# Optimization experiments

Hardware: AMD Instinct MI355X
Metric: run time of the kernel (lower is better)

The kernel has to match this reference:

```python
import jax, jax.numpy as jnp
import numpy as np

# SGCN (AsynSpiGCN) internals are not in the source; reconstructed as a standard
# LIF spiking-GCN: per time step, spikes propagate along edges weighted by
# edge_attr (gather src -> scatter-add dst), membrane potential decays with
# decay_alpha, neurons fire above threshold unless refractory, reset to v_r.
V_REST = 0.0
V_R = 0.0
SPEED = 1.0
THRESH = 0.5
REFRAC = 2.0
DECAY = 0.8
T_STEPS = 8
BETA = 0.5

N_NODES = 50000
N_EDGES = 800000
IN_DIM = 256
HID_DIM = 128


def setup_inputs() -> dict:
    key = jax.random.key(0)
    k1, k2, k3, k4, k5 = jax.random.split(key, 5)
    x = jax.random.normal(k1, (N_NODES, IN_DIM), dtype=jnp.float32)
    spike_node = jax.random.randint(k2, (N_NODES,), 0, 2, dtype=jnp.int32)
    edge_index = jax.random.randint(k3, (2, N_EDGES), 0, N_NODES, dtype=jnp.int32)
    node_indices = jnp.arange(N_NODES, dtype=jnp.int32)
    edge_attr = jax.random.uniform(k4, (N_EDGES,), dtype=jnp.float32)
    W = jax.random.normal(k5, (IN_DIM, HID_DIM), dtype=jnp.float32) * 0.05
    b = jnp.zeros((HID_DIM,), dtype=jnp.float32)
    return {"x": x, "spike_node": spike_node, "edge_index": edge_index,
            "node_indices": node_indices, "edge_attr": edge_attr, "W": W, "b": b}


def reference(x, spike_node, edge_index, node_indices, edge_attr, W, b):
    N = x.shape[0]
    # Linear projection + per-feature min-max standardization over nodes (dim 0)
    h = x @ W + b
    mn = h.min(axis=0, keepdims=True)
    mx = h.max(axis=0, keepdims=True)
    h = (h - mn) / (mx - mn + 1e-6)

    src, dst = edge_index[0], edge_index[1]
    v0 = jnp.full_like(h, V_REST)            # membrane potential [N, H]
    ref0 = jnp.zeros_like(h)                 # refractory counters [N, H]
    s0 = jnp.broadcast_to(spike_node.astype(h.dtype)[:, None], h.shape)

    def step(carry, _):
        v, ref, s = carry
        msg = s[src] * edge_attr[:, None]                      # [E, H] gather
        agg = jax.ops.segment_sum(msg, dst, num_segments=N)    # [N, H] scatter-add
        v = DECAY * v + SPEED * h + agg
        can_fire = ref <= 0
        spk = ((v >= THRESH) & can_fire).astype(h.dtype)
        v = jnp.where(spk > 0, V_R, v)
        ref = jnp.where(spk > 0, REFRAC, jnp.maximum(ref - 1.0, 0.0))
        return (v, ref, spk), spk

    (vT, _, _), spike_matrix = jax.lax.scan(step, (v0, ref0, s0), None, length=T_STEPS)
    fusion_tensor = h + BETA * vT
    return fusion_tensor, spike_matrix
```

## Files before the change

kernel.cpp:

```cpp
#include <hip/hip_runtime.h>
#include <cstdint>

#define N_NODES 50000
#define N_EDGES 800000
#define IN_DIM  256
#define HID     128
#define T_STEPS 8

#define AG_LOAD(p)     __hip_atomic_load((p), __ATOMIC_RELAXED, __HIP_MEMORY_SCOPE_AGENT)
#define AG_STORE(p, v) __hip_atomic_store((p), (v), __ATOMIC_RELAXED, __HIP_MEMORY_SCOPE_AGENT)
#define AG_ADD(p, v)   __hip_atomic_fetch_add((p), (v), __ATOMIC_RELAXED, __HIP_MEMORY_SCOPE_AGENT)
#define AG_MIN(p, v)   __hip_atomic_fetch_min((p), (v), __ATOMIC_RELAXED, __HIP_MEMORY_SCOPE_AGENT)
#define AG_MAX(p, v)   __hip_atomic_fetch_max((p), (v), __ATOMIC_RELAXED, __HIP_MEMORY_SCOPE_AGENT)

typedef unsigned long long u64;

static __device__ __forceinline__ unsigned int enc_f(float f) {
    unsigned int u = __float_as_uint(f);
    return (u & 0x80000000u) ? ~u : (u | 0x80000000u);
}
static __device__ __forceinline__ float dec_f(unsigned int u) {
    unsigned int b = (u & 0x80000000u) ? (u ^ 0x80000000u) : ~u;
    return __uint_as_float(b);
}

static __device__ __forceinline__ void fbar(int* bar, int nblk, int t) {
    int* flags = bar;
    int* go    = bar + 1900;
    __syncthreads();
    if (blockIdx.x == 0) {
        if (threadIdx.x == 0) AG_STORE(&flags[0], t);
        for (;;) {
            int ok = 1;
            for (int i = (int)threadIdx.x; i < nblk; i += 256)
                ok &= (AG_LOAD(&flags[i]) >= t);
            if (__syncthreads_and(ok)) break;
            __builtin_amdgcn_s_sleep(1);
        }
        if (threadIdx.x == 0) AG_STORE(go, t);
    } else {
        if (threadIdx.x == 0) {
            AG_STORE(&flags[blockIdx.x], t);
            while (AG_LOAD(go) < t) __builtin_amdgcn_s_sleep(4);
        }
        __syncthreads();
    }
}

template<int TNPB, int TNSLOT, int TECAP, int TBCAP, int TMINW>
__global__ __launch_bounds__(256, TMINW) void k_mega3(
    const float* __restrict__ x,
    const int*   __restrict__ spike_node,
    const int*   __restrict__ esrc,
    const int*   __restrict__ edst,
    const float* __restrict__ eattr,
    const float* __restrict__ W,
    const float* __restrict__ b,
    int* cnt, int4* bucket,
    unsigned int* mn_e, unsigned int* mx_e,
    uint32_t* sbA, uint32_t* sbB,
    float* __restrict__ out,
    int* bar, int nblk)
{
    constexpr int GEMMW = 4096 + TNPB * 36 + 64;
    constexpr int POOLW = (TECAP * 6 > GEMMW) ? TECAP * 6 : GEMMW;

    __shared__ int      lrp[TNPB + 1];
    __shared__ uint32_t pool[POOLW];
    __shared__ uint32_t sbw[TNPB][4];

    int*      ed_src_l  = (int*)pool;
    float*    ed_attr_l = (float*)(pool + TECAP);
    uint32_t* ed_wds    = pool + 2 * TECAP;
    float*    Ws        = (float*)pool;
    float*    xs        = (float*)(pool + 4096);
    float*    red_mn    = (float*)pool;
    float*    red_mx    = (float*)(pool + 1024);
    int*      cnt_l     = (int*)sbw;

    const int tid = threadIdx.x;
    const int bid = blockIdx.x;
    const int g   = tid >> 5, ln = tid & 31;
    const int n0  = bid * TNPB;
    const int ncnt = min(TNPB, N_NODES - n0);
    const int w = ln >> 3, shb = (ln & 7) * 4;
    const size_t NH = (size_t)N_NODES * HID;

    for (int i = tid; i < ncnt; i += 256) {
        uint32_t f = spike_node[n0 + i] ? 0xFFFFFFFFu : 0u;
        u64 ff = (u64)f | ((u64)f << 32);
        AG_STORE((u64*)&sbA[(size_t)(n0 + i) * 4], ff);
        AG_STORE((u64*)&sbA[(size_t)(n0 + i) * 4 + 2], ff);
    }

    for (int e = bid * 256 + tid; e < N_EDGES; e += nblk * 256) {
        int d = edst[e];
        int p = AG_ADD(&cnt[d], 1);
        if (p < TBCAP) {
            u64* qp = (u64*)&bucket[(size_t)d * TBCAP + p];
            u64 a  = (u64)(unsigned int)e | ((u64)(unsigned int)esrc[e] << 32);
            u64 bq = (u64)__float_as_uint(eattr[e]);
            AG_STORE(qp, a);
            AG_STORE(qp + 1, bq);
        }
    }

    float4 hs[TNSLOT], vs[TNSLOT];
    uint32_t rcs[TNSLOT], nibs[TNSLOT];
    #pragma unroll
    for (int s = 0; s < TNSLOT; ++s) hs[s] = make_float4(0.f, 0.f, 0.f, 0.f);
    int xoff[TNSLOT];
    #pragma unroll
    for (int s = 0; s < TNSLOT; ++s) xoff[s] = min(s * 8 + g, TNPB - 1) * 36;

    for (int kc = 0; kc < IN_DIM; kc += 32) {
        __syncthreads();
        for (int idx = tid; idx < TNPB * 8; idx += 256) {
            int node = idx >> 3, q = idx & 7;
            int row = min(n0 + node, N_NODES - 1);
            *(float4*)&xs[node * 36 + q * 4] =
                *(const float4*)(x + (size_t)row * IN_DIM + kc + q * 4);
        }
        for (int idx = tid; idx < 1024; idx += 256) {
            int r = idx >> 5, c = idx & 31;
            *(float4*)&Ws[r * 128 + c * 4] =
                *(const float4*)(W + (size_t)(kc + r) * HID + c * 4);
        }
        __syncthreads();
        #pragma unroll 4
        for (int k = 0; k < 32; ++k) {
            float4 wf = *(float4*)&Ws[k * 128 + ln * 4];
            #pragma unroll
            for (int s = 0; s < TNSLOT; ++s) {
                float xv = xs[xoff[s] + k];
                hs[s].x = __fmaf_rn(xv, wf.x, hs[s].x);
                hs[s].y = __fmaf_rn(xv, wf.y, hs[s].y);
                hs[s].z = __fmaf_rn(xv, wf.z, hs[s].z);
                hs[s].w = __fmaf_rn(xv, wf.w, hs[s].w);
            }
        }
    }
    {
        float4 bv = *(const float4*)(b + ln * 4);
        float lmn[4], lmx[4];
        #pragma unroll
        for (int c = 0; c < 4; ++c) { lmn[c] = INFINITY; lmx[c] = -INFINITY; }
        #pragma unroll
        for (int s = 0; s < TNSLOT; ++s) {
            hs[s].x = __fadd_rn(hs[s].x, bv.x);
            hs[s].y = __fadd_rn(hs[s].y, bv.y);
            hs[s].z = __fadd_rn(hs[s].z, bv.z);
            hs[s].w = __fadd_rn(hs[s].w, bv.w);
            lmn[0] = fminf(lmn[0], hs[s].x); lmx[0] = fmaxf(lmx[0], hs[s].x);
            lmn[1] = fminf(lmn[1], hs[s].y); lmx[1] = fmaxf(lmx[1], hs[s].y);
            lmn[2] = fminf(lmn[2], hs[s].z); lmx[2] = fmaxf(lmx[2], hs[s].z);
            lmn[3] = fminf(lmn[3], hs[s].w); lmx[3] = fmaxf(lmx[3], hs[s].w);
        }
        __syncthreads();
        #pragma unroll
        for (int c = 0; c < 4; ++c) {
            red_mn[g * 128 + ln * 4 + c] = lmn[c];
            red_mx[g * 128 + ln * 4 + c] = lmx[c];
        }
        __syncthreads();
        if (tid < 128) {
            float mnv = red_mn[tid], mxv = red_mx[tid];
            #pragma unroll
            for (int r = 1; r < 8; ++r) {
                mnv = fminf(mnv, red_mn[r * 128 + tid]);
                mxv = fmaxf(mxv, red_mx[r * 128 + tid]);
            }
            AG_MIN(&mn_e[tid], enc_f(mnv));
            AG_MAX(&mx_e[tid], enc_f(mxv));
        }
        __syncthreads();
    }

    fbar(bar, nblk, 1);

    if (tid < ncnt) cnt_l[tid] = min(AG_LOAD(&cnt[n0 + tid]), TBCAP);
    __syncthreads();
    if (tid == 0) {
        int run = 0;
        for (int i = 0; i < ncnt; ++i) { lrp[i] = run; run += cnt_l[i]; }
        lrp[ncnt] = run;
    }
    __syncthreads();
    const int etot  = lrp[ncnt];
    const bool inlds = (etot <= TECAP);

    {
        float mn0 = dec_f(AG_LOAD(&mn_e[ln * 4 + 0]));
        float mn1 = dec_f(AG_LOAD(&mn_e[ln * 4 + 1]));
        float mn2 = dec_f(AG_LOAD(&mn_e[ln * 4 + 2]));
        float mn3 = dec_f(AG_LOAD(&mn_e[ln * 4 + 3]));
        float dd0 = __fadd_rn(__fsub_rn(dec_f(AG_LOAD(&mx_e[ln * 4 + 0])), mn0), 1e-6f);
        float dd1 = __fadd_rn(__fsub_rn(dec_f(AG_LOAD(&mx_e[ln * 4 + 1])), mn1), 1e-6f);
        float dd2 = __fadd_rn(__fsub_rn(dec_f(AG_LOAD(&mx_e[ln * 4 + 2])), mn2), 1e-6f);
        float dd3 = __fadd_rn(__fsub_rn(dec_f(AG_LOAD(&mx_e[ln * 4 + 3])), mn3), 1e-6f);
        #pragma unroll
        for (int s = 0; s < TNSLOT; ++s) {
            hs[s].x = __fdiv_rn(__fsub_rn(hs[s].x, mn0), dd0);
            hs[s].y = __fdiv_rn(__fsub_rn(hs[s].y, mn1), dd1);
            hs[s].z = __fdiv_rn(__fsub_rn(hs[s].z, mn2), dd2);
            hs[s].w = __fdiv_rn(__fsub_rn(hs[s].w, mn3), dd3);
        }
    }
    #pragma unroll
    for (int s = 0; s < TNSLOT; ++s) { vs[s] = make_float4(0.f,0.f,0.f,0.f); rcs[s] = 0u; }

    if (inlds) {
        for (int m = tid >> 6; m < ncnt; m += 4) {
            int l = tid & 63;
            int lbeg = lrp[m];
            int c = lrp[m + 1] - lbeg;
            if (c <= 0) continue;
            const u64* brow = (const u64*)&bucket[(size_t)(n0 + m) * TBCAP];
            if (c <= 64) {
                int key = 0x7FFFFFFF, sv = 0, av = 0;
                if (l < c) {
                    u64 a  = AG_LOAD(brow + 2 * l);
                    u64 bq = AG_LOAD(brow + 2 * l + 1);
                    key = (int)(unsigned int)a;
                    sv  = (int)(unsigned int)(a >> 32);
                    av  = (int)(unsigned int)bq;
                }
                #pragma unroll
                for (int k = 2; k <= 64; k <<= 1) {
                    for (int j = k >> 1; j > 0; j >>= 1) {
                        int pk2 = __shfl_xor(key, j);
                        int ps  = __shfl_xor(sv, j);
                        int pa  = __shfl_xor(av, j);
                        bool lower = (l & j) == 0;
                        bool asc   = (l & k) == 0;
                        bool take  = (lower == asc) ? (pk2 < key) : (pk2 > key);
                        if (take) { key = pk2; sv = ps; av = pa; }
                    }
                }
                if (l < c) {
                    ed_src_l[lbeg + l]  = sv;
                    ed_attr_l[lbeg + l] = __int_as_float(av);
                }
            } else if (l == 0) {
                for (int i = 0; i < c; ++i) {
                    u64 a  = AG_LOAD(brow + 2 * i);
                    u64 bq = AG_LOAD(brow + 2 * i + 1);
                    int ke  = (int)(unsigned int)a;
                    int svv = (int)(unsigned int)(a >> 32);
                    int avv = (int)(unsigned int)bq;
                    int mm = i - 1;
                    while (mm >= 0 && (int)ed_wds[lbeg + mm] > ke) {
                        ed_wds[lbeg + mm + 1]    = ed_wds[lbeg + mm];
                        ed_src_l[lbeg + mm + 1]  = ed_src_l[lbeg + mm];
                        ed_attr_l[lbeg + mm + 1] = ed_attr_l[lbeg + mm];
                        --mm;
                    }
                    ed_wds[lbeg + mm + 1]    = (uint32_t)ke;
                    ed_src_l[lbeg + mm + 1]  = svv;
                    ed_attr_l[lbeg + mm + 1] = __int_as_float(avv);
                }
            }
        }
    } else {
        for (int m = tid >> 6; m < ncnt; m += 4) {
            int l = tid & 63;
            int c = lrp[m + 1] - lrp[m];
            if (c <= 1) continue;
            u64* brow = (u64*)&bucket[(size_t)(n0 + m) * TBCAP];
            if (c <= 64) {
                int key = 0x7FFFFFFF, sv = 0, av = 0;
                if (l < c) {
                    u64 a  = AG_LOAD(brow + 2 * l);
                    u64 bq = AG_LOAD(brow + 2 * l + 1);
                    key = (int)(unsigned int)a;
                    sv  = (int)(unsigned int)(a >> 32);
                    av  = (int)(unsigned int)bq;
                }
                #pragma unroll
                for (int k = 2; k <= 64; k <<= 1) {
                    for (int j = k >> 1; j > 0; j >>= 1) {
                        int pk2 = __shfl_xor(key, j);
                        int ps  = __shfl_xor(sv, j);
                        int pa  = __shfl_xor(av, j);
                        bool lower = (l & j) == 0;
                        bool asc   = (l & k) == 0;
                        bool take  = (lower == asc) ? (pk2 < key) : (pk2 > key);
                        if (take) { key = pk2; sv = ps; av = pa; }
                    }
                }
                if (l < c) {
                    u64 a = (u64)(unsigned int)key | ((u64)(unsigned int)sv << 32);
                    AG_STORE(brow + 2 * l, a);
                    AG_STORE(brow + 2 * l + 1, (u64)(unsigned int)av);
                }
            } else if (l == 0) {
                for (int i = 1; i < c; ++i) {
                    u64 ka = AG_LOAD(brow + 2 * i);
                    u64 kb = AG_LOAD(brow + 2 * i + 1);
                    int ke = (int)(unsigned int)ka;
                    int mm = i - 1;
                    while (mm >= 0) {
                        u64 ma = AG_LOAD(brow + 2 * mm);
                        if ((int)(unsigned int)ma <= ke) break;
                        AG_STORE(brow + 2 * mm + 2, ma);
                        AG_STORE(brow + 2 * mm + 3, AG_LOAD(brow + 2 * mm + 1));
                        --mm;
                    }
                    AG_STORE(brow + 2 * mm + 2, ka);
                    AG_STORE(brow + 2 * mm + 3, kb);
                }
            }
        }
    }
    __syncthreads();
    for (int i = tid; i < ncnt * 2; i += 256) ((u64*)sbw)[i] = 0ull;

    for (int t = 0; t < T_STEPS; ++t) {
        const uint32_t* cur = (t & 1) ? sbB : sbA;
        uint32_t*       nxt = (t & 1) ? sbA : sbB;
        if (t > 0) fbar(bar, nblk, 1 + t);

        if (inlds) {
            for (int i = tid; i < etot; i += 256) {
                u64* sp = (u64*)&cur[(size_t)ed_src_l[i] * 4];
                u64 lo = AG_LOAD(sp);
                u64 hi = AG_LOAD(sp + 1);
                uint4 wv;
                wv.x = (uint32_t)lo; wv.y = (uint32_t)(lo >> 32);
                wv.z = (uint32_t)hi; wv.w = (uint32_t)(hi >> 32);
                *(uint4*)&ed_wds[i * 4] = wv;
            }
        }
        __syncthreads();

        if (t > 0) {
            #pragma unroll
            for (int s = 0; s < TNSLOT; ++s) {
                int m = s * 8 + g;
                if (m < ncnt) {
                    uint32_t nb4 = nibs[s];
                    size_t idx = (size_t)(n0 + m) * HID + ln * 4;
                    *(float4*)&out[NH + (size_t)(t - 1) * NH + idx] = make_float4(
                        (nb4 & 1u) ? 1.0f : 0.0f, (nb4 & 2u) ? 1.0f : 0.0f,
                        (nb4 & 4u) ? 1.0f : 0.0f, (nb4 & 8u) ? 1.0f : 0.0f);
                }
            }
        }

        #pragma unroll
        for (int s = 0; s < TNSLOT; ++s) {
            int m = s * 8 + g;
            if (m < ncnt) {
                float ag0 = 0.f, ag1 = 0.f, ag2 = 0.f, ag3 = 0.f;
                if (inlds) {
                    int lb = lrp[m], le = lrp[m + 1];
                    for (int i = lb; i < le; ++i) {
                        uint32_t u = ed_wds[i * 4 + w];
                        float a = ed_attr_l[i];
                        uint32_t bits = (u >> shb) & 0xFu;
                        ag0 = __fadd_rn(ag0, (bits & 1u) ? a : 0.f);
                        ag1 = __fadd_rn(ag1, (bits & 2u) ? a : 0.f);
                        ag2 = __fadd_rn(ag2, (bits & 4u) ? a : 0.f);
                        ag3 = __fadd_rn(ag3, (bits & 8u) ? a : 0.f);
                    }
                } else {
                    int c = lrp[m + 1] - lrp[m];
                    const u64* brow = (const u64*)&bucket[(size_t)(n0 + m) * TBCAP];
                    for (int i = 0; i < c; ++i) {
                        u64 a  = AG_LOAD(brow + 2 * i);
                        u64 bq = AG_LOAD(brow + 2 * i + 1);
                        int srcn = (int)(unsigned int)(a >> 32);
                        float av = __uint_as_float((unsigned int)bq);
                        uint32_t u = AG_LOAD((uint32_t*)&cur[(size_t)srcn * 4 + w]);
                        uint32_t bits = (u >> shb) & 0xFu;
                        ag0 = __fadd_rn(ag0, (bits & 1u) ? av : 0.f);
                        ag1 = __fadd_rn(ag1, (bits & 2u) ? av : 0.f);
                        ag2 = __fadd_rn(ag2, (bits & 4u) ? av : 0.f);
                        ag3 = __fadd_rn(ag3, (bits & 8u) ? av : 0.f);
                    }
                }

                float hv[4] = {hs[s].x, hs[s].y, hs[s].z, hs[s].w};
                float vv[4] = {vs[s].x, vs[s].y, vs[s].z, vs[s].w};
                float ag[4] = {ag0, ag1, ag2, ag3};
                float vf[4];
                uint32_t rcu = rcs[s], rcn = 0u, nib = 0u;
                #pragma unroll
                for (int q = 0; q < 4; ++q) {
                    float vn = __fadd_rn(__fadd_rn(__fmul_rn(0.8f, vv[q]), hv[q]), ag[q]);
                    uint32_t rc = (rcu >> (8 * q)) & 0xFFu;
                    bool spk = (vn >= 0.5f) && (rc == 0u);
                    vf[q] = spk ? 0.0f : vn;
                    uint32_t rnew = spk ? 2u : (rc > 0u ? rc - 1u : 0u);
                    rcn |= rnew << (8 * q);
                    nib |= (spk ? 1u : 0u) << q;
                }
                vs[s] = make_float4(vf[0], vf[1], vf[2], vf[3]);
                rcs[s] = rcn;
                nibs[s] = nib;
                atomicOr(&sbw[m][w], nib << shb);
            }
        }
        __syncthreads();
        for (int i = tid; i < ncnt * 2; i += 256) {
            AG_STORE((u64*)&nxt[(size_t)n0 * 4] + i, ((u64*)sbw)[i]);
            ((u64*)sbw)[i] = 0ull;
        }
    }

    #pragma unroll
    for (int s = 0; s < TNSLOT; ++s) {
        int m = s * 8 + g;
        if (m < ncnt) {
            uint32_t nb4 = nibs[s];
            size_t idx = (size_t)(n0 + m) * HID + ln * 4;
            *(float4*)&out[NH + (size_t)(T_STEPS - 1) * NH + idx] = make_float4(
                (nb4 & 1u) ? 1.0f : 0.0f, (nb4 & 2u) ? 1.0f : 0.0f,
                (nb4 & 4u) ? 1.0f : 0.0f, (nb4 & 8u) ? 1.0f : 0.0f);
            *(float4*)&out[idx] = make_float4(
                __fadd_rn(hs[s].x, __fmul_rn(0.5f, vs[s].x)),
                __fadd_rn(hs[s].y, __fmul_rn(0.5f, vs[s].y)),
                __fadd_rn(hs[s].z, __fmul_rn(0.5f, vs[s].z)),
                __fadd_rn(hs[s].w, __fmul_rn(0.5f, vs[s].w)));
        }
    }
}

__global__ void k_count(const int* __restrict__ dst, int* __restrict__ counts) {
    int e = blockIdx.x * blockDim.x + threadIdx.x;
    if (e < N_EDGES) atomicAdd(&counts[dst[e]], 1);
}

__global__ void k_scan1(const int* __restrict__ counts, int* __restrict__ row_tmp,
                        int* __restrict__ blocksum) {
    __shared__ int sh[256];
    int t = threadIdx.x, i = blockIdx.x * 256 + t;
    int c = (i < N_NODES) ? counts[i] : 0;
    sh[t] = c; __syncthreads();
    for (int off = 1; off < 256; off <<= 1) {
        int val = (t >= off) ? sh[t - off] : 0;
        __syncthreads();
        sh[t] += val;
        __syncthreads();
    }
    if (i < N_NODES) row_tmp[i] = sh[t] - c;
    if (t == 255) blocksum[blockIdx.x] = sh[255];
}

__global__ void k_scan2(const int* __restrict__ blocksum, int* __restrict__ blockoff,
                        int nb, int* __restrict__ row_ptr) {
    if (threadIdx.x == 0) {
        int acc = 0;
        for (int b = 0; b < nb; ++b) { blockoff[b] = acc; acc += blocksum[b]; }
        row_ptr[N_NODES] = acc;
    }
}

__global__ void k_scan3(const int* __restrict__ row_tmp, const int* __restrict__ blockoff,
                        int* __restrict__ row_ptr) {
    int i = blockIdx.x * blockDim.x + threadIdx.x;
    if (i < N_NODES) row_ptr[i] = row_tmp[i] + blockoff[i >> 8];
}

__global__ void k_fill(const int* __restrict__ dst, const int* __restrict__ src,
                       const float* __restrict__ attr,
                       const int* __restrict__ row_ptr, int* __restrict__ cursor,
                       int* __restrict__ eid, int2* __restrict__ edata) {
    int e = blockIdx.x * blockDim.x + threadIdx.x;
    if (e >= N_EDGES) return;
    int d = dst[e];
    int p = row_ptr[d] + atomicAdd(&cursor[d], 1);
    eid[p]   = e;
    edata[p] = make_int2(src[e], __float_as_int(attr[e]));
}

__global__ __launch_bounds__(256) void k_bsort(const int* __restrict__ row_ptr,
                                               int* __restrict__ eid,
                                               int2* __restrict__ edata) {
    int node = blockIdx.x * 4 + (threadIdx.x >> 6);
    int l = threadIdx.x & 63;
    int beg = row_ptr[node], end = row_ptr[node + 1], cnt = end - beg;
    if (cnt <= 1) return;
    if (cnt <= 64) {
        int key = 0x7FFFFFFF, sv = 0, av = 0;
        if (l < cnt) { key = eid[beg + l]; int2 d = edata[beg + l]; sv = d.x; av = d.y; }
        #pragma unroll
        for (int k = 2; k <= 64; k <<= 1) {
            for (int j = k >> 1; j > 0; j >>= 1) {
                int pk = __shfl_xor(key, j);
                int ps = __shfl_xor(sv, j);
                int pa = __shfl_xor(av, j);
                bool lower = (l & j) == 0;
                bool asc   = (l & k) == 0;
                bool take = ((lower == asc)) ? (pk < key) : (pk > key);
                if (take) { key = pk; sv = ps; av = pa; }
            }
        }
        if (l < cnt) { eid[beg + l] = key; edata[beg + l] = make_int2(sv, av); }
    } else if (l == 0) {
        for (int i = beg + 1; i < end; ++i) {
            int ke = eid[i]; int2 kd = edata[i];
            int m = i - 1;
            while (m >= beg && eid[m] > ke) {
                eid[m+1] = eid[m]; edata[m+1] = edata[m]; --m;
            }
            eid[m+1] = ke; edata[m+1] = kd;
        }
    }
}

__global__ __launch_bounds__(256) void k_gemm(const float* __restrict__ x,
                                              const float* __restrict__ W,
                                              const float* __restrict__ b,
                                              float* __restrict__ h,
                                              unsigned int* __restrict__ mn_e,
                                              unsigned int* __restrict__ mx_e) {
    __shared__ float Ws[32 * 128];
    __shared__ float xs[64 * 36];
    __shared__ float red_mn[8 * 128];
    __shared__ float red_mx[8 * 128];
    const int tid = threadIdx.x;
    const int n0 = blockIdx.x * 64;
    const int jt = tid & 31, nt = tid >> 5;
    const int j0 = jt * 4;

    float acc[8][4];
    #pragma unroll
    for (int a = 0; a < 8; ++a)
        #pragma unroll
        for (int c = 0; c < 4; ++c) acc[a][c] = 0.0f;

    const int ldn = tid >> 2;
    const int kq  = (tid & 3) * 8;
    const int xrow = (n0 + ldn < N_NODES) ? (n0 + ldn) : (N_NODES - 1);
    const float* xg = x + (size_t)xrow * IN_DIM;

    for (int kc = 0; kc < IN_DIM; kc += 32) {
        __syncthreads();
        float4 xa = *(const float4*)(xg + kc + kq);
        float4 xb = *(const float4*)(xg + kc + kq + 4);
        *(float4*)&xs[ldn * 36 + kq]     = xa;
        *(float4*)&xs[ldn * 36 + kq + 4] = xb;
        #pragma unroll
        for (int p = 0; p < 4; ++p) {
            int r = nt + p * 8;
            *(float4*)&Ws[r * 128 + j0] =
                *(const float4*)(W + (size_t)(kc + r) * HID + j0);
        }
        __syncthreads();
        const float* xbase = &xs[nt * 8 * 36];
        #pragma unroll 4
        for (int k = 0; k < 32; ++k) {
            float4 wf = *(const float4*)&Ws[k * 128 + j0];
            #pragma unroll
            for (int ni = 0; ni < 8; ++ni) {
                float xv = xbase[ni * 36 + k];
                acc[ni][0] = __fmaf_rn(xv, wf.x, acc[ni][0]);
                acc[ni][1] = __fmaf_rn(xv, wf.y, acc[ni][1]);
                acc[ni][2] = __fmaf_rn(xv, wf.z, acc[ni][2]);
                acc[ni][3] = __fmaf_rn(xv, wf.w, acc[ni][3]);
            }
        }
    }

    float4 bv = *(const float4*)(b + j0);
    float lmn[4], lmx[4];
    #pragma unroll
    for (int c = 0; c < 4; ++c) { lmn[c] = INFINITY; lmx[c] = -INFINITY; }
    #pragma unroll
    for (int ni = 0; ni < 8; ++ni) {
        acc[ni][0] = __fadd_rn(acc[ni][0], bv.x);
        acc[ni][1] = __fadd_rn(acc[ni][1], bv.y);
        acc[ni][2] = __fadd_rn(acc[ni][2], bv.z);
        acc[ni][3] = __fadd_rn(acc[ni][3], bv.w);
        #pragma unroll
        for (int c = 0; c < 4; ++c) {
            lmn[c] = fminf(lmn[c], acc[ni][c]);
            lmx[c] = fmaxf(lmx[c], acc[ni][c]);
        }
    }
    #pragma unroll
    for (int c = 0; c < 4; ++c) {
        red_mn[nt * 128 + j0 + c] = lmn[c];
        red_mx[nt * 128 + j0 + c] = lmx[c];
    }
    __syncthreads();
    if (tid < 128) {
        float mnv = red_mn[tid], mxv = red_mx[tid];
        #pragma unroll
        for (int r = 1; r < 8; ++r) {
            mnv = fminf(mnv, red_mn[r * 128 + tid]);
            mxv = fmaxf(mxv, red_mx[r * 128 + tid]);
        }
        atomicMin(&mn_e[tid], enc_f(mnv));
        atomicMax(&mx_e[tid], enc_f(mxv));
    }
    #pragma unroll
    for (int ni = 0; ni < 8; ++ni) {
        int n = n0 + nt * 8 + ni;
        if (n < N_NODES)
            *(float4*)&h[(size_t)n * HID + j0] =
                make_float4(acc[ni][0], acc[ni][1], acc[ni][2], acc[ni][3]);
    }
}

__global__ void k_init_bits(const int* __restrict__ spike_node, uint32_t* __restrict__ sb) {
    int n = blockIdx.x * blockDim.x + threadIdx.x;
    if (n >= N_NODES) return;
    uint32_t f = spike_node[n] ? 0xFFFFFFFFu : 0u;
    sb[(size_t)n * 4 + 0] = f;
    sb[(size_t)n * 4 + 1] = f;
    sb[(size_t)n * 4 + 2] = f;
    sb[(size_t)n * 4 + 3] = f;
}

__global__ __launch_bounds__(128) void k_step(const int* __restrict__ row_ptr,
                                              const int2* __restrict__ edata,
                                              const uint32_t* __restrict__ sb_cur,
                                              uint32_t* __restrict__ sb_nxt,
                                              float* __restrict__ h,
                                              float* __restrict__ v,
                                              unsigned char* __restrict__ refc,
                                              const unsigned int* __restrict__ mn_e,
                                              const unsigned int* __restrict__ mx_e,
                                              float* __restrict__ out_spk,
                                              float* __restrict__ out_fus,
                                              int t0, int is_last) {
    __shared__ float    attr_l[4][128];
    __shared__ uint32_t words_l[4][128][4];
    __shared__ uint32_t sbw[16];
    __shared__ int      rp[5];

    const int tid = threadIdx.x;
    const int ns = tid >> 5, ln = tid & 31;
    const int nb = blockIdx.x * 4;
    const int n  = nb + ns;

    if (tid < 16) sbw[tid] = 0;
    if (tid < 5)  rp[tid] = row_ptr[nb + tid];
    __syncthreads();

    const int beg = rp[ns], cnt = rp[ns + 1] - beg;
    int cmax = 0;
    #pragma unroll
    for (int q = 0; q < 4; ++q) cmax = max(cmax, rp[q + 1] - rp[q]);
    const int nchunk = (cmax + 127) >> 7;

    float agg0 = 0.f, agg1 = 0.f, agg2 = 0.f, agg3 = 0.f;
    const int w = ln >> 3, shb = (ln & 7) * 4;

    for (int ch = 0; ch < nchunk; ++ch) {
        int base = ch << 7;
        __syncthreads();
        #pragma unroll
        for (int rep = 0; rep < 4; ++rep) {
            int i = base + rep * 32 + ln;
            if (i < cnt) {
                int2 d = edata[beg + i];
                attr_l[ns][rep * 32 + ln] = __int_as_float(d.y);
                *(uint4*)&words_l[ns][rep * 32 + ln][0] =
                    *(const uint4*)&sb_cur[(size_t)d.x * 4];
            }
        }
        __syncthreads();
        int lim = min(128, cnt - base);
        for (int i = 0; i < lim; ++i) {
            uint32_t u = words_l[ns][i][w];
            float a = attr_l[ns][i];
            uint32_t bits = (u >> shb) & 0xFu;
            agg0 = __fadd_rn(agg0, (bits & 1u) ? a : 0.0f);
            agg1 = __fadd_rn(agg1, (bits & 2u) ? a : 0.0f);
            agg2 = __fadd_rn(agg2, (bits & 4u) ? a : 0.0f);
            agg3 = __fadd_rn(agg3, (bits & 8u) ? a : 0.0f);
        }
    }

    const size_t idx = (size_t)n * HID + ln * 4;
    float4 h4 = *(const float4*)&h[idx];
    if (t0) {
        const int jb = ln * 4;
        float hq[4] = {h4.x, h4.y, h4.z, h4.w};
        #pragma unroll
        for (int q = 0; q < 4; ++q) {
            float mn = dec_f(mn_e[jb + q]);
            float mx = dec_f(mx_e[jb + q]);
            float d2 = __fadd_rn(__fsub_rn(mx, mn), 1e-6f);
            hq[q] = __fdiv_rn(__fsub_rn(hq[q], mn), d2);
        }
        h4 = make_float4(hq[0], hq[1], hq[2], hq[3]);
        *(float4*)&h[idx] = h4;
    }
    float4 v4;
    unsigned int rcu;
    if (t0) { v4 = make_float4(0.f, 0.f, 0.f, 0.f); rcu = 0u; }
    else    { v4 = *(const float4*)&v[idx]; rcu = *(const unsigned int*)&refc[idx]; }

    float hv[4]  = {h4.x, h4.y, h4.z, h4.w};
    float vv[4]  = {v4.x, v4.y, v4.z, v4.w};
    float ag[4]  = {agg0, agg1, agg2, agg3};
    float vf[4], sf[4];
    unsigned int rcn = 0u, nib = 0u;
    #pragma unroll
    for (int q = 0; q < 4; ++q) {
        float vn = __fadd_rn(__fadd_rn(__fmul_rn(0.8f, vv[q]), hv[q]), ag[q]);
        unsigned int rc = (rcu >> (8 * q)) & 0xFFu;
        bool spk = (vn >= 0.5f) && (rc == 0u);
        vf[q] = spk ? 0.0f : vn;
        sf[q] = spk ? 1.0f : 0.0f;
        unsigned int rnew = spk ? 2u : (rc > 0u ? rc - 1u : 0u);
        rcn |= rnew << (8 * q);
        nib |= (spk ? 1u : 0u) << q;
    }
    *(float4*)&v[idx] = make_float4(vf[0], vf[1], vf[2], vf[3]);
    *(unsigned int*)&refc[idx] = rcn;
    *(float4*)&out_spk[idx] = make_float4(sf[0], sf[1], sf[2], sf[3]);
    if (is_last) {
        *(float4*)&out_fus[idx] = make_float4(
            __fadd_rn(hv[0], __fmul_rn(0.5f, vf[0])),
            __fadd_rn(hv[1], __fmul_rn(0.5f, vf[1])),
            __fadd_rn(hv[2], __fmul_rn(0.5f, vf[2])),
            __fadd_rn(hv[3], __fmul_rn(0.5f, vf[3])));
    }
    atomicOr(&sbw[ns * 4 + w], nib << shb);
    __syncthreads();
    if (tid < 16)
        sb_nxt[(size_t)(nb + (tid >> 2)) * 4 + (tid & 3)] = sbw[tid];
}

extern "C" void kernel_launch(void* const* d_in, const int* in_sizes, int n_in,
                              void* d_out, int out_size, void* d_ws, size_t ws_size,
                              hipStream_t stream) {
    const float* x          = (const float*)d_in[0];
    const int*   spike_node = (const int*)  d_in[1];
    const int*   edge_index = (const int*)  d_in[2];
    const float* edge_attr  = (const float*)d_in[4];
    const float* W          = (const float*)d_in[5];
    const float* b          = (const float*)d_in[6];
    float* out = (float*)d_out;

    const int* src = edge_index;
    const int* dst = edge_index + N_EDGES;

    char* wsp = (char*)d_ws;
    auto alloc = [&](size_t bytes) {
        char* p = wsp;
        wsp += (bytes + 255) & ~(size_t)255;
        return p;
    };

    const int NB = (N_NODES + 255) / 256;
    const int EB = (N_EDGES + 255) / 256;
    const size_t NH = (size_t)N_NODES * HID;
    const int BCAP = 80;

    auto kC = k_mega3<33, 5, 768, 80, 6>;
    auto kE = k_mega3<50, 7, 1152, 80, 4>;
    auto kA = k_mega3<66, 9, 1536, 80, 3>;
    int occC = 0, occE = 0, occA = 0;
    hipOccupancyMaxActiveBlocksPerMultiprocessor(&occC, kC, 256, 0);
    hipOccupancyMaxActiveBlocksPerMultiprocessor(&occE, kE, 256, 0);
    hipOccupancyMaxActiveBlocksPerMultiprocessor(&occA, kA, 256, 0);

    if (occC >= 6 || occE >= 4 || occA >= 3) {
        int4*         bucket = (int4*)        alloc((size_t)N_NODES * BCAP * 16);
        int*          cnt    = (int*)         alloc((size_t)N_NODES * 4);
        uint32_t*     sbA    = (uint32_t*)    alloc((size_t)N_NODES * 16);
        uint32_t*     sbB    = (uint32_t*)    alloc((size_t)N_NODES * 16);
        unsigned int* mn_e   = (unsigned int*)alloc(HID * 4);
        unsigned int* mx_e   = (unsigned int*)alloc(HID * 4);
        int*          barv   = (int*)         alloc(8192);

        hipMemsetAsync(cnt,  0x00, (size_t)N_NODES * 4, stream);
        hipMemsetAsync(mn_e, 0xFF, HID * 4, stream);
        hipMemsetAsync(mx_e, 0x00, HID * 4, stream);
        hipMemsetAsync(barv, 0x00, 8192, stream);

        if (occC >= 6) {
            const int grid = (N_NODES + 32) / 33;
            kC<<<grid, 256, 0, stream>>>(x, spike_node, src, dst, edge_attr, W, b,
                                         cnt, bucket, mn_e, mx_e, sbA, sbB,
                                         out, barv, grid);
        } else if (occE >= 4) {
            const int grid = (N_NODES + 49) / 50;
            kE<<<grid, 256, 0, stream>>>(x, spike_node, src, dst, edge_attr, W, b,
                                         cnt, bucket, mn_e, mx_e, sbA, sbB,
                                         out, barv, grid);
        } else {
            const int grid = (N_NODES + 65) / 66;
            kA<<<grid, 256, 0, stream>>>(x, spike_node, src, dst, edge_attr, W, b,
                                         cnt, bucket, mn_e, mx_e, sbA, sbB,
                                         out, barv, grid);
        }
        return;
    }

    float*         h        = (float*)        alloc((size_t)N_NODES * HID * 4);
    float*         v        = (float*)        alloc((size_t)N_NODES * HID * 4);
    unsigned char* refc     = (unsigned char*)alloc((size_t)N_NODES * HID);
    uint32_t*      sbA      = (uint32_t*)     alloc((size_t)N_NODES * 16);
    uint32_t*      sbB      = (uint32_t*)     alloc((size_t)N_NODES * 16);
    int*           counts   = (int*)          alloc((size_t)N_NODES * 4);
    int*           cursor   = (int*)          alloc((size_t)N_NODES * 4);
    int*           row_tmp  = (int*)          alloc((size_t)N_NODES * 4);
    int*           row_ptr  = (int*)          alloc((size_t)(N_NODES + 1) * 4);
    int*           blocksum = (int*)          alloc(1024 * 4);
    int*           blockoff = (int*)          alloc(1024 * 4);
    int*           eid      = (int*)          alloc((size_t)N_EDGES * 4);
    int2*          edata    = (int2*)         alloc((size_t)N_EDGES * 8);
    unsigned int*  mn_e     = (unsigned int*) alloc(HID * 4);
    unsigned int*  mx_e     = (unsigned int*) alloc(HID * 4);

    hipMemsetAsync(counts, 0x00, (size_t)N_NODES * 4, stream);
    hipMemsetAsync(cursor, 0x00, (size_t)N_NODES * 4, stream);
    hipMemsetAsync(mn_e,   0xFF, HID * 4, stream);
    hipMemsetAsync(mx_e,   0x00, HID * 4, stream);

    k_count<<<EB, 256, 0, stream>>>(dst, counts);
    k_scan1<<<NB, 256, 0, stream>>>(counts, row_tmp, blocksum);
    k_scan2<<<1, 64, 0, stream>>>(blocksum, blockoff, NB, row_ptr);
    k_scan3<<<NB, 256, 0, stream>>>(row_tmp, blockoff, row_ptr);
    k_fill<<<EB, 256, 0, stream>>>(dst, src, edge_attr, row_ptr, cursor, eid, edata);
    k_bsort<<<N_NODES / 4, 256, 0, stream>>>(row_ptr, eid, edata);
    k_gemm<<<(N_NODES + 63) / 64, 256, 0, stream>>>(x, W, b, h, mn_e, mx_e);
    k_init_bits<<<NB, 256, 0, stream>>>(spike_node, sbA);

    for (int t = 0; t < T_STEPS; ++t) {
        uint32_t* cur = (t & 1) ? sbB : sbA;
        uint32_t* nxt = (t & 1) ? sbA : sbB;
        k_step<<<N_NODES / 4, 128, 0, stream>>>(row_ptr, edata, cur, nxt,
                                                h, v, refc, mn_e, mx_e,
                                                out + NH + (size_t)t * NH,
                                                out, (t == 0) ? 1 : 0,
                                                (t == T_STEPS - 1) ? 1 : 0);
    }
}
```

Baseline: 622.4 us.

## Replace per-step grid barrier with per-node ready tags and per-step spike buffers

Drops the global grid barrier between time steps. Each step now writes its spike bitmap to its own buffer and sets a per-node ready tag, and consumers spin only on the tags of the source nodes they read. The intent is to let blocks run ahead of one another instead of all waiting on the slowest block each step. The cost is more workspace (eight spike buffers, seven tag arrays and their memset) plus per-edge polling loads. The launch order also changes to prefer the largest-tile variant (66 nodes per block).

```diff
diff --git a/kernel.cpp b/kernel.cpp
--- a/kernel.cpp
+++ b/kernel.cpp
@@ -48,7 +48,7 @@
 }
 
 template<int TNPB, int TNSLOT, int TECAP, int TBCAP, int TMINW>
-__global__ __launch_bounds__(256, TMINW) void k_mega3(
+__global__ __launch_bounds__(256, TMINW) void k_mega4(
     const float* __restrict__ x,
     const int*   __restrict__ spike_node,
     const int*   __restrict__ esrc,
@@ -58,7 +58,8 @@
     const float* __restrict__ b,
     int* cnt, int4* bucket,
     unsigned int* mn_e, unsigned int* mx_e,
-    uint32_t* sbA, uint32_t* sbB,
+    uint32_t* sbuf,
+    uint32_t* tagv,
     float* __restrict__ out,
     int* bar, int nblk)
 {
@@ -84,13 +85,14 @@
     const int n0  = bid * TNPB;
     const int ncnt = min(TNPB, N_NODES - n0);
     const int w = ln >> 3, shb = (ln & 7) * 4;
-    const size_t NH = (size_t)N_NODES * HID;
+    const size_t NH  = (size_t)N_NODES * HID;
+    const size_t SBN = (size_t)N_NODES * 4;
 
     for (int i = tid; i < ncnt; i += 256) {
         uint32_t f = spike_node[n0 + i] ? 0xFFFFFFFFu : 0u;
         u64 ff = (u64)f | ((u64)f << 32);
-        AG_STORE((u64*)&sbA[(size_t)(n0 + i) * 4], ff);
-        AG_STORE((u64*)&sbA[(size_t)(n0 + i) * 4 + 2], ff);
+        AG_STORE((u64*)&sbuf[(size_t)(n0 + i) * 4], ff);
+        AG_STORE((u64*)&sbuf[(size_t)(n0 + i) * 4 + 2], ff);
     }
 
     for (int e = bid * 256 + tid; e < N_EDGES; e += nblk * 256) {
@@ -316,13 +318,17 @@
     for (int i = tid; i < ncnt * 2; i += 256) ((u64*)sbw)[i] = 0ull;
 
     for (int t = 0; t < T_STEPS; ++t) {
-        const uint32_t* cur = (t & 1) ? sbB : sbA;
-        uint32_t*       nxt = (t & 1) ? sbA : sbB;
-        if (t > 0) fbar(bar, nblk, 1 + t);
+        const uint32_t* cur = sbuf + (size_t)t * SBN;
+        uint32_t*       nxt = sbuf + (size_t)(t + 1) * SBN;
 
         if (inlds) {
+            const uint32_t* ptag = tagv + (size_t)(t > 0 ? t - 1 : 0) * N_NODES;
             for (int i = tid; i < etot; i += 256) {
-                u64* sp = (u64*)&cur[(size_t)ed_src_l[i] * 4];
+                int s = ed_src_l[i];
+                if (t > 0)
+                    while (AG_LOAD(&ptag[s]) == 0u)
+                        __builtin_amdgcn_s_sleep(1);
+                const u64* sp = (const u64*)&cur[(size_t)s * 4];
                 u64 lo = AG_LOAD(sp);
                 u64 hi = AG_LOAD(sp + 1);
                 uint4 wv;
@@ -371,7 +377,12 @@
                         u64 bq = AG_LOAD(brow + 2 * i + 1);
                         int srcn = (int)(unsigned int)(a >> 32);
                         float av = __uint_as_float((unsigned int)bq);
-                        uint32_t u = AG_LOAD((uint32_t*)&cur[(size_t)srcn * 4 + w]);
+                        if (t > 0) {
+                            const uint32_t* pt = tagv + (size_t)(t - 1) * N_NODES;
+                            while (AG_LOAD(&pt[srcn]) == 0u)
+                                __builtin_amdgcn_s_sleep(2);
+                        }
+                        uint32_t u = AG_LOAD(&cur[(size_t)srcn * 4 + w]);
                         uint32_t bits = (u >> shb) & 0xFu;
                         ag0 = __fadd_rn(ag0, (bits & 1u) ? av : 0.f);
                         ag1 = __fadd_rn(ag1, (bits & 2u) ? av : 0.f);
@@ -402,9 +413,14 @@
             }
         }
         __syncthreads();
-        for (int i = tid; i < ncnt * 2; i += 256) {
-            AG_STORE((u64*)&nxt[(size_t)n0 * 4] + i, ((u64*)sbw)[i]);
-            ((u64*)sbw)[i] = 0ull;
+        if (t < T_STEPS - 1) {
+            for (int i = tid; i < ncnt * 2; i += 256) {
+                AG_STORE((u64*)&nxt[(size_t)n0 * 4] + i, ((u64*)sbw)[i]);
+                ((u64*)sbw)[i] = 0ull;
+            }
+            __syncthreads();
+            for (int i = tid; i < ncnt; i += 256)
+                AG_STORE(&tagv[(size_t)t * N_NODES + n0 + i], 1u);
         }
     }
 
@@ -753,42 +769,43 @@
     const size_t NH = (size_t)N_NODES * HID;
     const int BCAP = 80;
 
-    auto kC = k_mega3<33, 5, 768, 80, 6>;
-    auto kE = k_mega3<50, 7, 1152, 80, 4>;
-    auto kA = k_mega3<66, 9, 1536, 80, 3>;
-    int occC = 0, occE = 0, occA = 0;
+    auto kA = k_mega4<66, 9, 1536, 80, 3>;
+    auto kC = k_mega4<33, 5, 768, 80, 6>;
+    auto kE = k_mega4<50, 7, 1152, 80, 4>;
+    int occA = 0, occC = 0, occE = 0;
+    hipOccupancyMaxActiveBlocksPerMultiprocessor(&occA, kA, 256, 0);
     hipOccupancyMaxActiveBlocksPerMultiprocessor(&occC, kC, 256, 0);
     hipOccupancyMaxActiveBlocksPerMultiprocessor(&occE, kE, 256, 0);
-    hipOccupancyMaxActiveBlocksPerMultiprocessor(&occA, kA, 256, 0);
-
-    if (occC >= 6 || occE >= 4 || occA >= 3) {
+
+    if (occA >= 3 || occC >= 6 || occE >= 4) {
         int4*         bucket = (int4*)        alloc((size_t)N_NODES * BCAP * 16);
         int*          cnt    = (int*)         alloc((size_t)N_NODES * 4);
-        uint32_t*     sbA    = (uint32_t*)    alloc((size_t)N_NODES * 16);
-        uint32_t*     sbB    = (uint32_t*)    alloc((size_t)N_NODES * 16);
+        uint32_t*     sbuf   = (uint32_t*)    alloc((size_t)N_NODES * 16 * 8);
+        uint32_t*     tagv   = (uint32_t*)    alloc((size_t)N_NODES * 4 * 7);
         unsigned int* mn_e   = (unsigned int*)alloc(HID * 4);
         unsigned int* mx_e   = (unsigned int*)alloc(HID * 4);
         int*          barv   = (int*)         alloc(8192);
 
         hipMemsetAsync(cnt,  0x00, (size_t)N_NODES * 4, stream);
+        hipMemsetAsync(tagv, 0x00, (size_t)N_NODES * 4 * 7, stream);
         hipMemsetAsync(mn_e, 0xFF, HID * 4, stream);
         hipMemsetAsync(mx_e, 0x00, HID * 4, stream);
         hipMemsetAsync(barv, 0x00, 8192, stream);
 
-        if (occC >= 6) {
+        if (occA >= 3) {
+            const int grid = (N_NODES + 65) / 66;
+            kA<<<grid, 256, 0, stream>>>(x, spike_node, src, dst, edge_attr, W, b,
+                                         cnt, bucket, mn_e, mx_e, sbuf, tagv,
+                                         out, barv, grid);
+        } else if (occC >= 6) {
             const int grid = (N_NODES + 32) / 33;
             kC<<<grid, 256, 0, stream>>>(x, spike_node, src, dst, edge_attr, W, b,
-                                         cnt, bucket, mn_e, mx_e, sbA, sbB,
+                                         cnt, bucket, mn_e, mx_e, sbuf, tagv,
                                          out, barv, grid);
-        } else if (occE >= 4) {
+        } else {
             const int grid = (N_NODES + 49) / 50;
             kE<<<grid, 256, 0, stream>>>(x, spike_node, src, dst, edge_attr, W, b,
-                                         cnt, bucket, mn_e, mx_e, sbA, sbB,
-                                         out, barv, grid);
-        } else {
-            const int grid = (N_NODES + 65) / 66;
-            kA<<<grid, 256, 0, stream>>>(x, spike_node, src, dst, edge_attr, W, b,
-                                         cnt, bucket, mn_e, mx_e, sbA, sbB,
+                                         cnt, bucket, mn_e, mx_e, sbuf, tagv,
                                          out, barv, grid);
         }
         return;
```

After: 623.9 us. No clear change (+0.2%).
